# Kernel tuning notes

Measured on AMD Instinct MI355X. Metric: run time of the kernel, lower is better.

## Reference

```python
import jax, jax.numpy as jnp
import numpy as np

B, N, DIM_IN, DIM_OUT, EMBED, CHEB_K = 32, 2000, 64, 64, 16, 3


def setup_inputs() -> dict:
    key = jax.random.key(0)
    ks = jax.random.split(key, 6)
    return {
        "x": jax.random.normal(ks[0], (B, N, DIM_IN), dtype=jnp.float32),
        "node_embeddings": jax.random.normal(ks[1], (N, EMBED), dtype=jnp.float32),
        "nodevec1": jax.random.normal(ks[2], (N, EMBED), dtype=jnp.float32),
        "nodevec2": jax.random.normal(ks[3], (EMBED, N), dtype=jnp.float32),
        "weights_pool": jax.random.normal(ks[4], (EMBED, CHEB_K, DIM_IN, DIM_OUT), dtype=jnp.float32) * 0.1,
        "bias_pool": jax.random.normal(ks[5], (EMBED, DIM_OUT), dtype=jnp.float32) * 0.1,
    }


def reference(x, node_embeddings, nodevec1, nodevec2, weights_pool, bias_pool):
    n = node_embeddings.shape[0]
    # adaptive adjacency: softmax(relu(nodevec1 @ nodevec2)) over rows' neighbors
    s = jax.nn.softmax(jax.nn.relu(nodevec1 @ nodevec2), axis=1)  # [N, N]
    # Chebyshev polynomial stack: T0 = I, T1 = S, Tk = 2 S Tk-1 - Tk-2
    support_set = [jnp.eye(n, dtype=x.dtype), s]
    for _ in range(2, CHEB_K):
        support_set.append(2.0 * s @ support_set[-1] - support_set[-2])
    supports = jnp.stack(support_set, axis=0)  # [K, N, N]
    # node-conditioned weights / bias
    weights = jnp.einsum('nd,dkio->nkio', node_embeddings, weights_pool)  # [N, K, I, O]
    bias = node_embeddings @ bias_pool  # [N, O]
    # graph conv: aggregate then per-node combine
    x_g = jnp.einsum('knm,bmc->bnkc', supports, x)  # [B, N, K, I]
    out = jnp.einsum('bnki,nkio->bno', x_g, weights) + bias  # [B, N, O]
    return out
```

## Files before the change

### kernel.cpp

```cpp
#include <hip/hip_runtime.h>

#define N_NODES 2000
#define NP      2048
#define KB      63
#define KB2     64
#define BATCH   32
#define DIM     64
#define EMB     16
#define KI      192
#define WCOLS   12288

typedef __bf16 bf16;
typedef __attribute__((ext_vector_type(8))) __bf16 bf16x8;
typedef __attribute__((ext_vector_type(4))) float  f32x4;

struct alignas(8) bf16x4pk { bf16 v[4]; };

__device__ __forceinline__ void gl_lds16(const bf16* g, bf16* l) {
    __builtin_amdgcn_global_load_lds(
        (__attribute__((address_space(1))) void*)(g),
        (__attribute__((address_space(3))) void*)(l), 16, 0, 0);
}


__global__ __launch_bounds__(256) void adj_softmax_pack(
    const float* __restrict__ nv1, const float* __restrict__ nv2,
    bf16* __restrict__ Sp)
{
    const int row = blockIdx.x;
    const int tid = threadIdx.x;
    const int j0  = tid * 8;
    __shared__ float sa[EMB];
    __shared__ float wred[4];
    __shared__ float bcast;
    if (tid < EMB) sa[tid] = nv1[row * EMB + tid];
    __syncthreads();

    const bool active = (tid < 250);
    float v[8] = {0,0,0,0,0,0,0,0};
    if (active) {
#pragma unroll
        for (int d = 0; d < EMB; ++d) {
            const float sd = sa[d];
            const float4 q0 = *(const float4*)&nv2[d * N_NODES + j0];
            const float4 q1 = *(const float4*)&nv2[d * N_NODES + j0 + 4];
            v[0] += sd * q0.x; v[1] += sd * q0.y; v[2] += sd * q0.z; v[3] += sd * q0.w;
            v[4] += sd * q1.x; v[5] += sd * q1.y; v[6] += sd * q1.z; v[7] += sd * q1.w;
        }
    }
    float lmax = 0.0f;
#pragma unroll
    for (int jj = 0; jj < 8; ++jj) { v[jj] = fmaxf(v[jj], 0.0f); lmax = fmaxf(lmax, v[jj]); }
#pragma unroll
    for (int off = 32; off > 0; off >>= 1)
        lmax = fmaxf(lmax, __shfl_down(lmax, off, 64));
    if ((tid & 63) == 0) wred[tid >> 6] = lmax;
    __syncthreads();
    if (tid == 0) bcast = fmaxf(fmaxf(wred[0], wred[1]), fmaxf(wred[2], wred[3]));
    __syncthreads();
    const float rmax = bcast;

    float lsum = 0.0f;
    if (active) {
#pragma unroll
        for (int jj = 0; jj < 8; ++jj) { v[jj] = __expf(v[jj] - rmax); lsum += v[jj]; }
    }
#pragma unroll
    for (int off = 32; off > 0; off >>= 1)
        lsum += __shfl_down(lsum, off, 64);
    if ((tid & 63) == 0) wred[tid >> 6] = lsum;
    __syncthreads();
    if (tid == 0) bcast = wred[0] + wred[1] + wred[2] + wred[3];
    __syncthreads();
    const float inv = 1.0f / bcast;

    if (tid < 252) {
        bf16x8 pk;
#pragma unroll
        for (int jj = 0; jj < 8; ++jj)
            pk[jj] = (bf16)(active ? v[jj] * inv : 0.0f);
        const int kb = j0 >> 5, q = (j0 >> 3) & 3;
        const int nt = row >> 6, r = row & 63;
        *(bf16x8*)&Sp[((size_t)(kb * 32 + nt) * 256 + q * 64 + r) * 8] = pk;
    }
}

__global__ __launch_bounds__(256) void transpose_pack_x(
    const float* __restrict__ X, bf16* __restrict__ Xtp, bf16* __restrict__ Xbf)
{
    const int b  = blockIdx.y;
    const int m0 = blockIdx.x * 64;
    const int tid = threadIdx.x;
    __shared__ bf16 T[64][72];
#pragma unroll
    for (int i = 0; i < 4; ++i) {
        int idx = i * 256 + tid;
        int r  = idx >> 4;
        int c4 = (idx & 15) * 4;
        int m  = m0 + r;
        float4 v = make_float4(0.f, 0.f, 0.f, 0.f);
        if (m < N_NODES)
            v = *(const float4*)&X[((size_t)b * N_NODES + m) * DIM + c4];
        bf16x4pk pk;
        pk.v[0] = (bf16)v.x; pk.v[1] = (bf16)v.y;
        pk.v[2] = (bf16)v.z; pk.v[3] = (bf16)v.w;
        if (m < N_NODES)
            *(bf16x4pk*)&Xbf[((size_t)b * N_NODES + m) * DIM + c4] = pk;
        T[c4 + 0][r] = pk.v[0];
        T[c4 + 1][r] = pk.v[1];
        T[c4 + 2][r] = pk.v[2];
        T[c4 + 3][r] = pk.v[3];
    }
    __syncthreads();
#pragma unroll
    for (int i = 0; i < 2; ++i) {
        int idx = i * 256 + tid;
        int c   = idx >> 3;
        int mch = idx & 7;
        int kb  = (m0 >> 5) + (mch >> 2);
        if (kb < KB) {
            int q = mch & 3;
            bf16x8 vv = *(const bf16x8*)&T[c][mch * 8];
            *(bf16x8*)&Xtp[((size_t)(b * KB2 + kb) * 256 + q * 64 + c) * 8] = vv;
        }
    }
}

__global__ __launch_bounds__(64) void spmm_pack(
    const bf16* __restrict__ Ap, const bf16* __restrict__ Btp,
    bf16* __restrict__ Ybf, bf16* __restrict__ Ytp, int write_ytp)
{
    const int nt = blockIdx.x;
    const int b  = blockIdx.y;
    const int n0 = nt * 64;
    const int lane = threadIdx.x;
    const int l15 = lane & 15, quad = lane >> 4;

    __shared__ bf16 sta[4][2048];
    __shared__ bf16 stb[4][2048];

    const bf16* asrc = Ap  + (size_t)nt * 2048 + lane * 8;
    const bf16* bsrc = Btp + (size_t)(b * KB2) * 2048 + lane * 8;

#define DMA_STAGE(st, kb_) {                                         \
        const bf16* pa = asrc + (size_t)(kb_) * (32 * 2048);         \
        const bf16* pb = bsrc + (size_t)(kb_) * 2048;                \
        gl_lds16(pa,        &sta[st][lane * 8]);                     \
        gl_lds16(pa + 512,  &sta[st][ 512 + lane * 8]);              \
        gl_lds16(pa + 1024, &sta[st][1024 + lane * 8]);              \
        gl_lds16(pa + 1536, &sta[st][1536 + lane * 8]);              \
        gl_lds16(pb,        &stb[st][lane * 8]);                     \
        gl_lds16(pb + 512,  &stb[st][ 512 + lane * 8]);              \
        gl_lds16(pb + 1024, &stb[st][1024 + lane * 8]);              \
        gl_lds16(pb + 1536, &stb[st][1536 + lane * 8]); }

    f32x4 acc[4][4] = {};

    DMA_STAGE(0, 0); DMA_STAGE(1, 1); DMA_STAGE(2, 2);

#pragma unroll 1
    for (int kb = 0; kb < KB2; ++kb) {
        const int s = kb & 3;
        bf16x8 af[4], bfr[4];
#pragma unroll
        for (int t = 0; t < 4; ++t)
            af[t]  = *(const bf16x8*)&sta[s][(quad * 64 + t * 16 + l15) * 8];
#pragma unroll
        for (int t = 0; t < 4; ++t)
            bfr[t] = *(const bf16x8*)&stb[s][(quad * 64 + t * 16 + l15) * 8];
        if (kb < KB2 - 3) DMA_STAGE((kb + 3) & 3, kb + 3);
#pragma unroll
        for (int rt = 0; rt < 4; ++rt)
#pragma unroll
            for (int ct = 0; ct < 4; ++ct)
                acc[rt][ct] = __builtin_amdgcn_mfma_f32_16x16x32_bf16(
                    af[rt], bfr[ct], acc[rt][ct], 0, 0, 0);
    }
#undef DMA_STAGE

#pragma unroll
    for (int rt = 0; rt < 4; ++rt) {
        const int nbase = n0 + rt * 16 + quad * 4;
#pragma unroll
        for (int ct = 0; ct < 4; ++ct) {
            const int c = ct * 16 + l15;
#pragma unroll
            for (int r = 0; r < 4; ++r) {
                int n = nbase + r;
                if (n < N_NODES)
                    Ybf[((size_t)b * N_NODES + n) * DIM + c] = (bf16)acc[rt][ct][r];
            }
            if (write_ytp && nbase + 4 <= N_NODES) {
                const int kb2 = nbase >> 5;
                const int m5  = nbase & 31;
                const int kq  = m5 >> 3;
                const int j4  = m5 & 7;
                bf16x4pk pk;
                pk.v[0] = (bf16)acc[rt][ct][0];
                pk.v[1] = (bf16)acc[rt][ct][1];
                pk.v[2] = (bf16)acc[rt][ct][2];
                pk.v[3] = (bf16)acc[rt][ct][3];
                *(bf16x4pk*)&Ytp[((size_t)(b * KB2 + kb2) * 256 + kq * 64 + c) * 8 + j4] = pk;
            }
        }
    }
}

#define Z0   (WCOLS * 32)
#define Z1   (Z0 + N_NODES * 32)
#define Z2   (Z1 + NP * 32)
__global__ __launch_bounds__(256) void prep_small(
    const float* __restrict__ wp, const float* __restrict__ emb,
    bf16* __restrict__ wpT2, bf16* __restrict__ embp, bf16* __restrict__ Sp63)
{
    int idx = blockIdx.x * 256 + threadIdx.x;
    if (idx < Z0) {
        int col = idx >> 5, d = idx & 31;
        int o  = col / KI;
        int kk = col - o * KI;
        int cheb = kk >> 6, i = kk & 63;
        float v = (d < EMB) ? wp[(((d * 3 + cheb) * 64 + i) * 64) + o] : 0.0f;
        wpT2[idx] = (bf16)v;
    } else if (idx < Z1) {
        int j = idx - Z0;
        int n = j >> 5, d = j & 31;
        float v = (d < EMB) ? emb[n * EMB + d] : 0.0f;
        embp[j] = (bf16)v;
    } else if (idx < Z2) {
        Sp63[idx - Z1] = (bf16)0.0f;
    }
}

__global__ __launch_bounds__(256) void prep_W_mfma(
    const bf16* __restrict__ embp, const bf16* __restrict__ wpT2,
    bf16* __restrict__ W)
{
    const int colbase = blockIdx.x * 256;
    const int n0      = blockIdx.y * 16;
    const int tid  = threadIdx.x;
    const int lane = tid & 63, wave = tid >> 6;
    const int l15 = lane & 15, quad = lane >> 4;

    __shared__ bf16 Cs[16][264];

    const bf16x8 af = *(const bf16x8*)&embp[(n0 + l15) * 32 + quad * 8];
    const f32x4 zero = {};
#pragma unroll
    for (int ct = 0; ct < 4; ++ct) {
        const int col = colbase + wave * 64 + ct * 16 + l15;
        bf16x8 bfr = *(const bf16x8*)&wpT2[(size_t)col * 32 + quad * 8];
        f32x4 acc = __builtin_amdgcn_mfma_f32_16x16x32_bf16(af, bfr, zero, 0, 0, 0);
#pragma unroll
        for (int r = 0; r < 4; ++r)
            Cs[quad * 4 + r][wave * 64 + ct * 16 + l15] = (bf16)acc[r];
    }
    __syncthreads();
    {
        const int row = tid >> 4;
        const int c16 = (tid & 15) * 16;
        bf16x8 v0 = *(const bf16x8*)&Cs[row][c16];
        bf16x8 v1 = *(const bf16x8*)&Cs[row][c16 + 8];
        bf16* dst = &W[(size_t)(n0 + row) * WCOLS + colbase + c16];
        *(bf16x8*)dst       = v0;
        *(bf16x8*)(dst + 8) = v1;
    }
}

__global__ __launch_bounds__(256) void combine_node(
    const bf16* __restrict__ xbf, const bf16* __restrict__ y1bf,
    const bf16* __restrict__ y2bf, const float* __restrict__ emb,
    const float* __restrict__ bp, const bf16* __restrict__ W,
    float* __restrict__ out)
{
    const int n   = blockIdx.x;
    const int tid = threadIdx.x;
    const int lane = tid & 63, wave = tid >> 6;
    const int l15 = lane & 15, quad = lane >> 4;

    __shared__ bf16 As[BATCH][200];
    __shared__ bf16 Ws[DIM][200];
    __shared__ float bias_s[DIM];
    __shared__ float emb_s[EMB];

    if (tid < EMB) emb_s[tid] = emb[n * EMB + tid];

    {
        const int b  = tid >> 3;
        const int c8 = (tid & 7) * 8;
        const size_t base = ((size_t)b * N_NODES + n) * DIM + c8;
        bf16x8 vx = *(const bf16x8*)&xbf [base];
        bf16x8 v1 = *(const bf16x8*)&y1bf[base];
        bf16x8 v2 = *(const bf16x8*)&y2bf[base];
        bf16x8 p2;
#pragma unroll
        for (int e = 0; e < 8; ++e)
            p2[e] = (bf16)(2.0f * (float)v2[e] - (float)vx[e]);
        *(bf16x8*)&As[b][c8]       = vx;
        *(bf16x8*)&As[b][64 + c8]  = v1;
        *(bf16x8*)&As[b][128 + c8] = p2;
    }
    {
        const bf16* Wn = W + (size_t)n * WCOLS;
#pragma unroll
        for (int jj = 0; jj < 6; ++jj) {
            int chunk = jj * 256 + tid;
            int o  = chunk / 24;
            int kc = chunk - o * 24;
            bf16x8 v = *(const bf16x8*)&Wn[(size_t)chunk * 8];
            *(bf16x8*)&Ws[o][kc * 8] = v;
        }
    }
    __syncthreads();

    if (tid < DIM) {
        float s = 0.0f;
#pragma unroll
        for (int d = 0; d < EMB; ++d) s += emb_s[d] * bp[d * DIM + tid];
        bias_s[tid] = s;
    }

    bf16x8 af[2][6];
#pragma unroll
    for (int mt = 0; mt < 2; ++mt)
#pragma unroll
        for (int ks = 0; ks < 6; ++ks)
            af[mt][ks] = *(const bf16x8*)&As[mt * 16 + l15][ks * 32 + quad * 8];

    f32x4 acc[2] = {};
#pragma unroll
    for (int ks = 0; ks < 6; ++ks) {
        bf16x8 bfr = *(const bf16x8*)&Ws[wave * 16 + l15][ks * 32 + quad * 8];
        acc[0] = __builtin_amdgcn_mfma_f32_16x16x32_bf16(af[0][ks], bfr, acc[0], 0, 0, 0);
        acc[1] = __builtin_amdgcn_mfma_f32_16x16x32_bf16(af[1][ks], bfr, acc[1], 0, 0, 0);
    }
    __syncthreads();

    const int o = wave * 16 + l15;
    const float bv = bias_s[o];
#pragma unroll
    for (int mt = 0; mt < 2; ++mt)
#pragma unroll
        for (int r = 0; r < 4; ++r) {
            int b = mt * 16 + quad * 4 + r;
            out[((size_t)b * N_NODES + n) * DIM + o] = acc[mt][r] + bv;
        }
}

extern "C" void kernel_launch(void* const* d_in, const int* in_sizes, int n_in,
                              void* d_out, int out_size, void* d_ws, size_t ws_size,
                              hipStream_t stream) {
    const float* x   = (const float*)d_in[0];
    const float* emb = (const float*)d_in[1];
    const float* nv1 = (const float*)d_in[2];
    const float* nv2 = (const float*)d_in[3];
    const float* wp  = (const float*)d_in[4];
    const float* bp  = (const float*)d_in[5];
    float* out = (float*)d_out;

    char* w = (char*)d_ws;
    bf16* Sp   = (bf16*)w;  w += (size_t)KB2 * NP * 32 * 2;
    bf16* xTp  = (bf16*)w;  w += (size_t)BATCH * KB2 * DIM * 32 * 2;
    bf16* y1Tp = (bf16*)w;  w += (size_t)BATCH * KB2 * DIM * 32 * 2;
    bf16* xbf  = (bf16*)w;  w += (size_t)BATCH * N_NODES * DIM * 2;
    bf16* y1bf = (bf16*)w;  w += (size_t)BATCH * N_NODES * DIM * 2;
    bf16* y2bf = (bf16*)w;  w += (size_t)BATCH * N_NODES * DIM * 2;
    bf16* wpT2 = (bf16*)w;  w += (size_t)WCOLS * 32 * 2;
    bf16* embp = (bf16*)w;  w += (size_t)N_NODES * 32 * 2;
    bf16* W    = (bf16*)w;

    adj_softmax_pack<<<N_NODES, 256, 0, stream>>>(nv1, nv2, Sp);
    transpose_pack_x<<<dim3(32, BATCH), 256, 0, stream>>>(x, xTp, xbf);
    prep_small<<<(Z2 + 255) / 256, 256, 0, stream>>>(
        wp, emb, wpT2, embp, Sp + (size_t)63 * NP * 32);
    prep_W_mfma<<<dim3(WCOLS / 256, N_NODES / 16), 256, 0, stream>>>(embp, wpT2, W);
    spmm_pack<<<dim3(32, BATCH), 64, 0, stream>>>(Sp, xTp,  y1bf, y1Tp, 1);
    spmm_pack<<<dim3(32, BATCH), 64, 0, stream>>>(Sp, y1Tp, y2bf, y1Tp, 0);
    combine_node<<<N_NODES, 256, 0, stream>>>(xbf, y1bf, y2bf, emb, bp, W, out);
}
```

Baseline: 192.9 us.

## Restructure spmm into four-wave 128-row blocks with shared double-buffered LDS tiles

The dense S·X product kernel moves from single-wave blocks (64 rows each, four-stage async LDS pipeline) to 256-thread blocks of four waves that together cover 128 rows. Each B tile loaded into LDS is now shared by all four waves, and each wave computes a 32x64 output tile. The pipeline drops to two LDS buffers with a block barrier every k-step. The aim is to halve redundant B tile loads and improve latency hiding through more cooperating waves. In exchange, each wave does less MFMA work per step, prefetch depth is shallower, and a barrier is added every iteration.

```diff
diff --git a/kernel.cpp b/kernel.cpp
--- a/kernel.cpp
+++ b/kernel.cpp
@@ -126,61 +126,59 @@
     }
 }
 
-__global__ __launch_bounds__(64) void spmm_pack(
+__global__ __launch_bounds__(256, 2) void spmm_pack(
     const bf16* __restrict__ Ap, const bf16* __restrict__ Btp,
     bf16* __restrict__ Ybf, bf16* __restrict__ Ytp, int write_ytp)
 {
-    const int nt = blockIdx.x;
-    const int b  = blockIdx.y;
-    const int n0 = nt * 64;
-    const int lane = threadIdx.x;
+    const int ntB = blockIdx.x;
+    const int b   = blockIdx.y;
+    const int n0  = ntB * 128;
+    const int tid = threadIdx.x;
+    const int lane = tid & 63, wave = tid >> 6;
     const int l15 = lane & 15, quad = lane >> 4;
 
-    __shared__ bf16 sta[4][2048];
-    __shared__ bf16 stb[4][2048];
-
-    const bf16* asrc = Ap  + (size_t)nt * 2048 + lane * 8;
-    const bf16* bsrc = Btp + (size_t)(b * KB2) * 2048 + lane * 8;
-
-#define DMA_STAGE(st, kb_) {                                         \
-        const bf16* pa = asrc + (size_t)(kb_) * (32 * 2048);         \
-        const bf16* pb = bsrc + (size_t)(kb_) * 2048;                \
-        gl_lds16(pa,        &sta[st][lane * 8]);                     \
-        gl_lds16(pa + 512,  &sta[st][ 512 + lane * 8]);              \
-        gl_lds16(pa + 1024, &sta[st][1024 + lane * 8]);              \
-        gl_lds16(pa + 1536, &sta[st][1536 + lane * 8]);              \
-        gl_lds16(pb,        &stb[st][lane * 8]);                     \
-        gl_lds16(pb + 512,  &stb[st][ 512 + lane * 8]);              \
-        gl_lds16(pb + 1024, &stb[st][1024 + lane * 8]);              \
-        gl_lds16(pb + 1536, &stb[st][1536 + lane * 8]); }
-
-    f32x4 acc[4][4] = {};
-
-    DMA_STAGE(0, 0); DMA_STAGE(1, 1); DMA_STAGE(2, 2);
-
+    __shared__ bf16 As[2][4096];
+    __shared__ bf16 Bs[2][2048];
+
+    const bf16* aslab = Ap  + (size_t)(ntB * 2) * 2048 + tid * 8;
+    const bf16* bslab = Btp + (size_t)(b * KB2) * 2048 + tid * 8;
+
+#define DMA_KB(buf, kb_) {                                           \
+        const bf16* pa = aslab + (size_t)(kb_) * (32 * 2048);        \
+        const bf16* pb = bslab + (size_t)(kb_) * 2048;               \
+        gl_lds16(pa,        &As[buf][tid * 8]);                      \
+        gl_lds16(pa + 2048, &As[buf][2048 + tid * 8]);               \
+        gl_lds16(pb,        &Bs[buf][tid * 8]);  }
+
+    f32x4 acc[2][4] = {};
+    const int ga = (wave >> 1) * 256 + quad * 64 + (wave & 1) * 32;
+    const int gb = quad * 64;
+
+    DMA_KB(0, 0);
 #pragma unroll 1
     for (int kb = 0; kb < KB2; ++kb) {
-        const int s = kb & 3;
-        bf16x8 af[4], bfr[4];
+        const int cur = kb & 1;
+        __syncthreads();
+        bf16x8 af[2], bfr[4];
+#pragma unroll
+        for (int t = 0; t < 2; ++t)
+            af[t]  = *(const bf16x8*)&As[cur][(ga + t * 16 + l15) * 8];
 #pragma unroll
         for (int t = 0; t < 4; ++t)
-            af[t]  = *(const bf16x8*)&sta[s][(quad * 64 + t * 16 + l15) * 8];
-#pragma unroll
-        for (int t = 0; t < 4; ++t)
-            bfr[t] = *(const bf16x8*)&stb[s][(quad * 64 + t * 16 + l15) * 8];
-        if (kb < KB2 - 3) DMA_STAGE((kb + 3) & 3, kb + 3);
-#pragma unroll
-        for (int rt = 0; rt < 4; ++rt)
+            bfr[t] = *(const bf16x8*)&Bs[cur][(gb + t * 16 + l15) * 8];
+        if (kb + 1 < KB2) DMA_KB(cur ^ 1, kb + 1);
+#pragma unroll
+        for (int rt = 0; rt < 2; ++rt)
 #pragma unroll
             for (int ct = 0; ct < 4; ++ct)
                 acc[rt][ct] = __builtin_amdgcn_mfma_f32_16x16x32_bf16(
                     af[rt], bfr[ct], acc[rt][ct], 0, 0, 0);
     }
-#undef DMA_STAGE
-
-#pragma unroll
-    for (int rt = 0; rt < 4; ++rt) {
-        const int nbase = n0 + rt * 16 + quad * 4;
+#undef DMA_KB
+
+#pragma unroll
+    for (int rt = 0; rt < 2; ++rt) {
+        const int nbase = n0 + wave * 32 + rt * 16 + quad * 4;
 #pragma unroll
         for (int ct = 0; ct < 4; ++ct) {
             const int c = ct * 16 + l15;
@@ -192,9 +190,8 @@
             }
             if (write_ytp && nbase + 4 <= N_NODES) {
                 const int kb2 = nbase >> 5;
-                const int m5  = nbase & 31;
-                const int kq  = m5 >> 3;
-                const int j4  = m5 & 7;
+                const int kq  = (nbase & 31) >> 3;
+                const int j4  = nbase & 7;
                 bf16x4pk pk;
                 pk.v[0] = (bf16)acc[rt][ct][0];
                 pk.v[1] = (bf16)acc[rt][ct][1];
@@ -373,7 +370,7 @@
     prep_small<<<(Z2 + 255) / 256, 256, 0, stream>>>(
         wp, emb, wpT2, embp, Sp + (size_t)63 * NP * 32);
     prep_W_mfma<<<dim3(WCOLS / 256, N_NODES / 16), 256, 0, stream>>>(embp, wpT2, W);
-    spmm_pack<<<dim3(32, BATCH), 64, 0, stream>>>(Sp, xTp,  y1bf, y1Tp, 1);
-    spmm_pack<<<dim3(32, BATCH), 64, 0, stream>>>(Sp, y1Tp, y2bf, y1Tp, 0);
+    spmm_pack<<<dim3(16, BATCH), 256, 0, stream>>>(Sp, xTp,  y1bf, y1Tp, 1);
+    spmm_pack<<<dim3(16, BATCH), 256, 0, stream>>>(Sp, y1Tp, y2bf, y1Tp, 0);
     combine_node<<<N_NODES, 256, 0, stream>>>(xbf, y1bf, y2bf, emb, bp, W, out);
 }
```

Result: no change. 191.0 us (-1.0%).
